# Optimization experiments

Hardware: AMD Instinct MI355X
Metric: run time of the kernel (lower is better)

## Reference

```python
import jax, jax.numpy as jnp
import numpy as np

N, K, M, DIN, DOUT = 4096, 16, 65536, 256, 256


def setup_inputs() -> dict:
    key = jax.random.key(0)
    ks = jax.random.split(key, 16)
    s = 1.0 / np.sqrt(DOUT)
    x = jax.random.normal(ks[0], (N, DIN), jnp.float32)
    h_tensor = jax.random.normal(ks[1], (M, DOUT), jnp.float32)
    c_tensor = jax.random.normal(ks[2], (M, DOUT), jnp.float32)
    # variable-length child lists: lengths in [1, K], -1 padding like get_nums()
    lengths = jax.random.randint(ks[3], (N,), 1, K + 1)
    idx = jax.random.randint(ks[4], (N, K), 0, M)
    t = jnp.arange(K)[None, :]
    indice = jnp.where(t < lengths[:, None], idx, -1).astype(jnp.int32)
    W_w = jax.random.normal(ks[5], (4 * DOUT, DIN), jnp.float32) * s
    W_b = jax.random.normal(ks[6], (4 * DOUT,), jnp.float32) * s
    h0 = jax.random.normal(ks[7], (4, DOUT), jnp.float32)
    c0 = jax.random.normal(ks[8], (4, DOUT), jnp.float32)
    Wih = jax.random.normal(ks[9], (4, 2, 4 * DOUT, DOUT), jnp.float32) * s
    Whh = jax.random.normal(ks[10], (4, 2, 4 * DOUT, DOUT), jnp.float32) * s
    bih = jax.random.normal(ks[11], (4, 2, 4 * DOUT), jnp.float32) * s
    bhh = jax.random.normal(ks[12], (4, 2, 4 * DOUT), jnp.float32) * s
    fc = jax.random.normal(ks[13], (4, DOUT, 2 * DOUT), jnp.float32) * s
    return dict(x=x, h_tensor=h_tensor, c_tensor=c_tensor, indice=indice,
                W_w=W_w, W_b=W_b, h0=h0, c0=c0, Wih=Wih, Whh=Whh,
                bih=bih, bhh=bhh, fc=fc)


def _lstm_dir(xseq, mask, h_init, c_init, W_ih, W_hh, b, reverse):
    """Masked LSTM over child axis. xseq [N,K,d], mask [N,K] bool. Mimics
    pack_padded_sequence: state frozen and output 0 at padded steps."""
    d = h_init.shape[-1]
    xs = jnp.swapaxes(xseq, 0, 1)   # [K,N,d]
    ms = jnp.swapaxes(mask, 0, 1)   # [K,N]

    def step(carry, inp):
        h, c = carry
        xt, mt = inp
        g = xt @ W_ih.T + h @ W_hh.T + b        # [N,4d], gate order i,f,g,o
        i = jax.nn.sigmoid(g[:, :d])
        f = jax.nn.sigmoid(g[:, d:2 * d])
        u = jnp.tanh(g[:, 2 * d:3 * d])
        o = jax.nn.sigmoid(g[:, 3 * d:])
        c_new = f * c + i * u
        h_new = o * jnp.tanh(c_new)
        m = mt[:, None]
        return (jnp.where(m, h_new, h), jnp.where(m, c_new, c)), jnp.where(m, h_new, 0.0)

    _, ys = jax.lax.scan(step, (h_init, c_init), (xs, ms), reverse=reverse)
    return jnp.swapaxes(ys, 0, 1)   # [N,K,d]


def _bilstm_seq(xseq, mask, h0j, c0j, Wihj, Whhj, bihj, bhhj, fcj):
    n = xseq.shape[0]
    h_init = jnp.broadcast_to(h0j, (n, h0j.shape[-1]))
    c_init = jnp.broadcast_to(c0j, (n, c0j.shape[-1]))
    yf = _lstm_dir(xseq, mask, h_init, c_init, Wihj[0], Whhj[0], bihj[0] + bhhj[0], False)
    yb = _lstm_dir(xseq, mask, h_init, c_init, Wihj[1], Whhj[1], bihj[1] + bhhj[1], True)
    y = jnp.concatenate([yf, yb], axis=-1)      # [N,K,2d]
    return jnp.einsum('nkh,dh->nkd', y, fcj)    # fc (no bias); 0 stays 0 at pads


def reference(x, h_tensor, c_tensor, indice, W_w, W_b, h0, c0, Wih, Whh, bih, bhh, fc):
    mask = indice != -1                           # [N,K]
    length = mask.sum(axis=1)                     # [N], >= 1
    safe_idx = jnp.where(mask, indice, 0)
    h = h_tensor[safe_idx]                        # [N,K,d] gather of child states
    c = c_tensor[safe_idx]
    Wx = x @ W_w.T + W_b                          # [N,4d]
    d = DOUT
    Wf, Wi, Wu, Wo = Wx[:, :d], Wx[:, d:2 * d], Wx[:, 2 * d:3 * d], Wx[:, 3 * d:]
    ys = [_bilstm_seq(h, mask, h0[j], c0[j], Wih[j], Whh[j], bih[j], bhh[j], fc[j])
          for j in range(4)]                      # U_f, U_i, U_u, U_o
    # forget branch: per-child gate, masked sum over children
    branch_f_k = jax.nn.sigmoid(Wf[:, None, :] + ys[0])
    branch_f = jnp.sum(branch_f_k * c * mask[..., None], axis=1)
    # i/u/o use last valid timestep (packed LSTM y_last)
    ar = jnp.arange(x.shape[0])
    last = length - 1
    branch_i = jax.nn.sigmoid(ys[1][ar, last] + Wi)
    branch_u = jnp.tanh(ys[2][ar, last] + Wu)
    branch_o = jax.nn.sigmoid(ys[3][ar, last] + Wo)
    new_c = branch_i * branch_u + branch_f
    new_h = branch_o * jnp.tanh(new_c)
    return new_h, new_c
```

## Files before the change

kernel.cpp:

```cpp
#include <hip/hip_runtime.h>
#include <math.h>

#define N_SEQ 4096
#define KCH   16
#define DM    256
#define G4    1024
#define LP    40
#define EP    68

typedef __attribute__((ext_vector_type(8))) short bf8;
typedef __attribute__((ext_vector_type(4))) float f4;

__device__ __forceinline__ float fast_rcp(float x) { return __builtin_amdgcn_rcpf(x); }
__device__ __forceinline__ float sigf(float x)   { return fast_rcp(1.f + __expf(-x)); }
__device__ __forceinline__ float tanh_f(float x) { return 1.f - 2.f * fast_rcp(1.f + __expf(2.f * x)); }

__device__ __forceinline__ float bf2f(unsigned short u) {
    return __uint_as_float(((unsigned)u) << 16);
}
__device__ __forceinline__ unsigned short f2bf(float f) {
    unsigned u = __float_as_uint(f);
    unsigned r = (u + 0x7fffu + ((u >> 16) & 1u)) >> 16;
    return (unsigned short)r;
}
__device__ __forceinline__ unsigned pack2(float a, float b) {
    return (unsigned)f2bf(a) | ((unsigned)f2bf(b) << 16);
}

#define GLDS(gp, lp) __builtin_amdgcn_global_load_lds( \
    (const __attribute__((address_space(1))) void*)(gp), \
    (__attribute__((address_space(3))) void*)(lp), 16, 0, 0)

template<int NSEG, int LDB>
__device__ __forceinline__ void pass_pipe(
    const unsigned short* const (&segA)[NSEG],
    const unsigned short* const (&segB)[NSEG],
    unsigned short* SM,
    f4 (&acc)[4][4], int wave, int wm, int wn, int jq, int fr)
{
    unsigned short* const la[2] = { SM + wave * 1024,        SM + 8192 + wave * 1024 };
    unsigned short* const lb[2] = { SM + 4096 + wave * 1024, SM + 12288 + wave * 1024 };
    constexpr int NS = NSEG * 8;

    {
        const unsigned short* A_ = segA[0];
        const unsigned short* B_ = segB[0];
        GLDS(A_, la[0]);             GLDS(A_ + 16 * DM, la[0] + 512);
        GLDS(B_, lb[0]);             GLDS(B_ + 16 * LDB, lb[0] + 512);
    }
#pragma unroll
    for (int t = 0; t < NS; ++t) {
        if (t + 1 < NS) {
            const unsigned short* A_ = segA[(t + 1) >> 3] + ((t + 1) & 7) * 32;
            const unsigned short* B_ = segB[(t + 1) >> 3] + ((t + 1) & 7) * 32;
            const int nb = (t + 1) & 1;
            GLDS(A_, la[nb]);        GLDS(A_ + 16 * DM, la[nb] + 512);
            GLDS(B_, lb[nb]);        GLDS(B_ + 16 * LDB, lb[nb] + 512);
            asm volatile("s_waitcnt vmcnt(4)" ::: "memory");
        } else {
            asm volatile("s_waitcnt vmcnt(0)" ::: "memory");
        }
        __builtin_amdgcn_s_barrier();

        const unsigned short* Ab = SM + (t & 1) * 8192;
        const unsigned short* Bb = Ab + 4096;
        bf8 af[4], bb[4];
#pragma unroll
        for (int i = 0; i < 4; ++i)
            af[i] = *(const bf8*)(Ab + (wm + i * 16 + fr) * 32 + jq);
#pragma unroll
        for (int j = 0; j < 4; ++j)
            bb[j] = *(const bf8*)(Bb + (wn + j * 16 + fr) * 32 + jq);
#pragma unroll
        for (int i = 0; i < 4; ++i)
#pragma unroll
            for (int j = 0; j < 4; ++j)
                acc[i][j] = __builtin_amdgcn_mfma_f32_16x16x32_bf16(
                    af[i], bb[j], acc[i][j], 0, 0, 0);

        asm volatile("s_waitcnt lgkmcnt(0)" ::: "memory");
        __builtin_amdgcn_s_barrier();
    }
}

template<int KLEN>
__device__ __forceinline__ void pass_bf(
    const unsigned short* __restrict__ aRow,
    const unsigned short* __restrict__ bRow,
    unsigned short* Asm, unsigned short* Bsm, f4 (&acc)[4][4])
{
    const int tid  = threadIdx.x;
    const int kh   = (tid & 1) * 16;
    const int srow = tid >> 1;
    const int lane = tid & 63, wave = tid >> 6;
    const int wm = (wave >> 1) * 64, wn = (wave & 1) * 64;
    const int fr = lane & 15, fk = (lane >> 4) * 8;
    unsigned short* da = Asm + srow * LP + kh;
    unsigned short* db = Bsm + srow * LP + kh;

    for (int k0 = 0; k0 < KLEN; k0 += 32) {
        __syncthreads();
        *(int4*)(da)     = *(const int4*)(aRow + k0 + kh);
        *(int4*)(da + 8) = *(const int4*)(aRow + k0 + kh + 8);
        *(int4*)(db)     = *(const int4*)(bRow + k0 + kh);
        *(int4*)(db + 8) = *(const int4*)(bRow + k0 + kh + 8);
        __syncthreads();
        bf8 af[4], bb[4];
#pragma unroll
        for (int i = 0; i < 4; ++i)
            af[i] = *(const bf8*)(Asm + (wm + i * 16 + fr) * LP + fk);
#pragma unroll
        for (int j = 0; j < 4; ++j)
            bb[j] = *(const bf8*)(Bsm + (wn + j * 16 + fr) * LP + fk);
#pragma unroll
        for (int i = 0; i < 4; ++i)
#pragma unroll
            for (int j = 0; j < 4; ++j)
                acc[i][j] = __builtin_amdgcn_mfma_f32_16x16x32_bf16(
                    af[i], bb[j], acc[i][j], 0, 0, 0);
    }
}

template<int KLEN>
__device__ __forceinline__ void pass_f32(
    const float* __restrict__ aRow,
    const unsigned short* __restrict__ bRow,
    unsigned short* Asm, unsigned short* Bsm, f4 (&acc)[4][4])
{
    const int tid  = threadIdx.x;
    const int kh   = (tid & 1) * 16;
    const int srow = tid >> 1;
    const int lane = tid & 63, wave = tid >> 6;
    const int wm = (wave >> 1) * 64, wn = (wave & 1) * 64;
    const int fr = lane & 15, fk = (lane >> 4) * 8;
    unsigned short* da = Asm + srow * LP + kh;
    unsigned short* db = Bsm + srow * LP + kh;

    for (int k0 = 0; k0 < KLEN; k0 += 32) {
        __syncthreads();
        {
            const float* s = aRow + k0 + kh;
            float4 v0 = *(const float4*)(s);
            float4 v1 = *(const float4*)(s + 4);
            float4 v2 = *(const float4*)(s + 8);
            float4 v3 = *(const float4*)(s + 12);
            *(int4*)(da)     = make_int4(pack2(v0.x, v0.y), pack2(v0.z, v0.w),
                                         pack2(v1.x, v1.y), pack2(v1.z, v1.w));
            *(int4*)(da + 8) = make_int4(pack2(v2.x, v2.y), pack2(v2.z, v2.w),
                                         pack2(v3.x, v3.y), pack2(v3.z, v3.w));
        }
        *(int4*)(db)     = *(const int4*)(bRow + k0 + kh);
        *(int4*)(db + 8) = *(const int4*)(bRow + k0 + kh + 8);
        __syncthreads();
        bf8 af[4], bb[4];
#pragma unroll
        for (int i = 0; i < 4; ++i)
            af[i] = *(const bf8*)(Asm + (wm + i * 16 + fr) * LP + fk);
#pragma unroll
        for (int j = 0; j < 4; ++j)
            bb[j] = *(const bf8*)(Bsm + (wn + j * 16 + fr) * LP + fk);
#pragma unroll
        for (int i = 0; i < 4; ++i)
#pragma unroll
            for (int j = 0; j < 4; ++j)
                acc[i][j] = __builtin_amdgcn_mfma_f32_16x16x32_bf16(
                    af[i], bb[j], acc[i][j], 0, 0, 0);
    }
}


__global__ __launch_bounds__(256) void k_lastidx(
    const int* __restrict__ indice, int* __restrict__ last_idx)
{
    const int n = blockIdx.x * 256 + threadIdx.x;
    if (n >= N_SEQ) return;
    int len = 0;
#pragma unroll
    for (int k = 0; k < KCH; ++k) len += (indice[n * KCH + k] != -1);
    last_idx[n] = indice[n * KCH + (len - 1)];
}

__global__ __launch_bounds__(1024) void k_hh0_bsum2(
    const float* __restrict__ bih, const float* __restrict__ bhh,
    const float* __restrict__ h0, const float* __restrict__ Whh,
    float* __restrict__ bsum2)
{
    const int jz = blockIdx.x, j = jz + 1;
    const int g = threadIdx.x;
    const int jd = j * 2 + 1;
    const float* wrow = Whh + ((size_t)jd * G4 + g) * DM;
    float s = bih[jd * G4 + g] + bhh[jd * G4 + g];
    for (int h = 0; h < DM; ++h) s = fmaf(h0[j * DM + h], wrow[h], s);
    const int c = (g & 255) * 4 + (g >> 8);
    bsum2[jz * G4 + c] = s;
}

__global__ __launch_bounds__(256) void k_init_states(
    const float* __restrict__ h0, const float* __restrict__ c0,
    unsigned short* __restrict__ hA, float* __restrict__ c_state)
{
    const int row = blockIdx.x;
    const int s = row >> 12;
    const int tree = (s < 4) ? s : 0;
    const int d = threadIdx.x;
    hA[(size_t)row * DM + d]      = f2bf(h0[tree * DM + d]);
    c_state[(size_t)row * DM + d] = c0[tree * DM + d];
}

__global__ __launch_bounds__(256) void k_zero4(float4* __restrict__ p)
{
    p[(size_t)blockIdx.x * 256 + threadIdx.x] = make_float4(0.f, 0.f, 0.f, 0.f);
}

__global__ __launch_bounds__(256) void k_prep_wcat(
    const float* __restrict__ Wih, const float* __restrict__ Whh,
    const float* __restrict__ bih, const float* __restrict__ bhh,
    unsigned short* __restrict__ wcat, float* __restrict__ bsumr)
{
    const int c = blockIdx.x, s = blockIdx.y;
    const int wsel = (s < 4) ? s * 2 : 1;
    const int d = c >> 2, g = c & 3;
    const size_t srcrow = ((size_t)wsel * G4 + g * DM + d) * DM;
    unsigned short* dst = wcat + ((size_t)s * G4 + c) * 512;
    const int t = threadIdx.x;
    dst[t]       = f2bf(Wih[srcrow + t]);
    dst[256 + t] = f2bf(Whh[srcrow + t]);
    if (t == 0)
        bsumr[s * G4 + c] = bih[wsel * G4 + g * DM + d] + bhh[wsel * G4 + g * DM + d];
}

__global__ __launch_bounds__(256) void k_prep_wcat2(
    const float* __restrict__ Wih, unsigned short* __restrict__ wcat2)
{
    const int c = blockIdx.x, jz = blockIdx.y, j = jz + 1;
    const int d = c >> 2, g = c & 3;
    const size_t srcrow = ((size_t)(j * 2 + 1) * G4 + g * DM + d) * DM;
    wcat2[((size_t)jz * G4 + c) * 256 + threadIdx.x] = f2bf(Wih[srcrow + threadIdx.x]);
}

__global__ __launch_bounds__(256) void k_prep_fcb(
    const float* __restrict__ fc, unsigned short* __restrict__ fcb)
{
    const int dout = blockIdx.x, z = blockIdx.y, t = threadIdx.x;
    fcb[((size_t)z * DM + dout) * DM + t] = f2bf(fc[(size_t)dout * 512 + z * DM + t]);
}

__global__ __launch_bounds__(256) void k_prep_fcb2(
    const float* __restrict__ fc, unsigned short* __restrict__ fcb2)
{
    const int dout = blockIdx.x, jz = blockIdx.y, j = jz + 1, t = threadIdx.x;
    const float* src = fc + ((size_t)j * DM + dout) * 512;
    unsigned short* dst = fcb2 + ((size_t)jz * DM + dout) * 512;
    dst[t]       = f2bf(src[t]);
    dst[t + 256] = f2bf(src[t + 256]);
}

__global__ __launch_bounds__(256) void k_prep_wwb(
    const float* __restrict__ W_w, unsigned short* __restrict__ wwb)
{
    const size_t i = (size_t)blockIdx.x * 256 + threadIdx.x;
    wwb[i] = f2bf(W_w[i]);
}

__device__ __forceinline__ void gather_slice(
    const float* __restrict__ h_tensor, const int* __restrict__ indice,
    unsigned short* __restrict__ xbuf, int zz, int kk, int blk)
{
    const int row = blk * 64 + (threadIdx.x >> 2);
    const int cb  = (threadIdx.x & 3) * 64;
    int idx = indice[row * KCH + kk]; if (idx < 0) idx = 0;
    const float* src = h_tensor + (size_t)idx * DM + cb;
    unsigned short* dst = xbuf + ((size_t)zz * N_SEQ + row) * DM + cb;
#pragma unroll
    for (int c = 0; c < 64; c += 4) {
        float4 v = *(const float4*)(src + c);
        *(uint2*)(dst + c) = make_uint2(pack2(v.x, v.y), pack2(v.z, v.w));
    }
}

__global__ __launch_bounds__(256) void k_gather_x0(
    const float* __restrict__ h_tensor, const int* __restrict__ indice,
    unsigned short* __restrict__ xbuf)
{
    const int slice = blockIdx.x >> 6, blk = blockIdx.x & 63;
    gather_slice(h_tensor, indice, xbuf, slice, slice ? (KCH - 1) : 0, blk);
}

__global__ __launch_bounds__(256) void k_scan_merged(
    const unsigned short* __restrict__ xb_cur, unsigned short* __restrict__ xb_nxt,
    const unsigned short* __restrict__ yb_prev, unsigned short* __restrict__ yb_cur,
    const int* __restrict__ indice, const float* __restrict__ h_tensor,
    const unsigned short* __restrict__ h_in, unsigned short* __restrict__ h_out,
    float* __restrict__ c_state,
    const unsigned short* __restrict__ wcat, const float* __restrict__ bsumr,
    const unsigned short* __restrict__ fcb, unsigned short* __restrict__ ys0,
    int r)
{
    __shared__ __align__(16) unsigned short SMEM[16384];

    const int tid  = threadIdx.x;
    const int lane = tid & 63, wave = tid >> 6;
    const int wm = (wave >> 1) * 64, wn = (wave & 1) * 64;
    const int fr = lane & 15;
    const int jq = ((lane >> 4) ^ ((fr >> 1) & 3)) * 8;
    const int lr = wave * 32 + (lane >> 2);
    const int jl = ((lane & 3) ^ ((lane >> 3) & 3)) * 8;

    const int bz = blockIdx.z;

    if (bz == 5) {
        const int id5 = blockIdx.x + 8 * blockIdx.y;
        if (id5 >= 128) {
            const int rr = r + 1;
            if (rr >= KCH) return;
            const int g = id5 - 128;
            const int zz = g >> 6;
            gather_slice(h_tensor, indice, xb_nxt, zz,
                         zz ? (KCH - 1 - rr) : rr, g & 63);
            return;
        }
        if (r == 0) return;
        const int rp = r - 1;
        const int z = id5 >> 6;
        const int kslice = z ? (KCH - 1 - rp) : rp;
        const int row0 = (id5 & 31) * 128;
        const int c0 = ((id5 >> 5) & 1) * 128;

        const unsigned short* ay0 = yb_prev + ((size_t)z * N_SEQ + row0 + lr) * DM + jl;
        const unsigned short* bf0 = fcb + ((size_t)z * DM + c0 + lr) * DM + jl;

        f4 acc[4][4];
#pragma unroll
        for (int i = 0; i < 4; ++i)
#pragma unroll
            for (int j = 0; j < 4; ++j) acc[i][j] = (f4)(0.f);
        {
            const unsigned short* const segA[1] = { ay0 };
            const unsigned short* const segB[1] = { bf0 };
            pass_pipe<1, 256>(segA, segB, SMEM, acc, wave, wm, wn, jq, fr);
        }

#pragma unroll
        for (int i = 0; i < 4; ++i)
#pragma unroll
            for (int j = 0; j < 4; ++j) {
                const int col = c0 + wn + j * 16 + fr;
#pragma unroll
                for (int reg = 0; reg < 4; ++reg) {
                    const int rowg = row0 + wm + i * 16 + (lane >> 4) * 4 + reg;
                    const size_t ix = ((size_t)rowg * KCH + kslice) * DM + col;
                    ys0[ix] = f2bf(bf2f(ys0[ix]) + acc[i][j][reg]);
                }
            }
        return;
    }

    const int s = bz;
    const int k = (s < 4) ? r : (KCH - 1 - r);
    const int z = (s < 4) ? 0 : 1;
    const int bn = blockIdx.y & 7;
    const int bm = (blockIdx.y >> 3) * 8 + blockIdx.x;
    const int row0 = bm * 128, c0 = bn * 128;

    const unsigned short* xz = xb_cur + (size_t)z * N_SEQ * DM;
    const unsigned short* hs_in = h_in + (size_t)s * N_SEQ * DM;
    const unsigned short* ax0 = xz + (size_t)(row0 + lr) * DM + jl;
    const unsigned short* ah0 = hs_in + (size_t)(row0 + lr) * DM + jl;
    const unsigned short* bw0 = wcat + ((size_t)s * G4 + c0 + lr) * 512 + jl;

    f4 acc[4][4];
#pragma unroll
    for (int i = 0; i < 4; ++i)
#pragma unroll
        for (int j = 0; j < 4; ++j) acc[i][j] = (f4)(0.f);

    {
        const unsigned short* const segA[2] = { ax0, ah0 };
        const unsigned short* const segB[2] = { bw0, bw0 + 256 };
        pass_pipe<2, 512>(segA, segB, SMEM, acc, wave, wm, wn, jq, fr);
    }

    float* sc = (float*)SMEM + wave * (16 * EP);
    __syncthreads();
#pragma unroll
    for (int i = 0; i < 4; ++i) {
#pragma unroll
        for (int j = 0; j < 4; ++j) {
            const int colL = j * 16 + fr;
            const int rbase = (lane >> 4) * 4;
#pragma unroll
            for (int reg = 0; reg < 4; ++reg)
                sc[(rbase + reg) * EP + colL] = acc[i][j][reg];
        }
        __syncthreads();
        const int rowg = row0 + wm + i * 16 + fr;
        const bool m = (indice[rowg * KCH + k] != -1);
#pragma unroll
        for (int q = 0; q < 4; ++q) {
            const int dL = (lane >> 4) + q * 4;
            const f4 gv = *(const f4*)(sc + fr * EP + dL * 4);
            const f4 bb = *(const f4*)(bsumr + s * G4 + c0 + wn + dL * 4);
            const int d = ((c0 + wn) >> 2) + dL;
            const float ii = sigf(gv.x + bb.x);
            const float ff = sigf(gv.y + bb.y);
            const float uu = tanh_f(gv.z + bb.z);
            const float oo = sigf(gv.w + bb.w);
            const size_t cix = ((size_t)s * N_SEQ + rowg) * DM + d;
            const float c_old = c_state[cix];
            const float cn = ff * c_old + ii * uu;
            const float cw = m ? cn : c_old;
            c_state[cix] = cw;
            const float hn = oo * tanh_f(cn);
            const unsigned short hv = m ? f2bf(hn) : hs_in[(size_t)rowg * DM + d];
            h_out[cix] = hv;
            if (s == 0)
                yb_cur[(size_t)rowg * DM + d] = m ? f2bf(hn) : (unsigned short)0;
            else if (s == 4)
                yb_cur[(size_t)(N_SEQ + rowg) * DM + d] = m ? f2bf(hn) : (unsigned short)0;
        }
        __syncthreads();
    }
}

__global__ __launch_bounds__(256) void k_acc_tail(
    const unsigned short* __restrict__ ybuf, const unsigned short* __restrict__ fcb,
    unsigned short* __restrict__ ys0)
{
    __shared__ __align__(16) unsigned short SMEM[16384];
    const int tid = threadIdx.x;
    const int lane = tid & 63, wave = tid >> 6;
    const int wm = (wave >> 1) * 64, wn = (wave & 1) * 64;
    const int fr = lane & 15;
    const int jq = ((lane >> 4) ^ ((fr >> 1) & 3)) * 8;
    const int lr = wave * 32 + (lane >> 2);
    const int jl = ((lane & 3) ^ ((lane >> 3) & 3)) * 8;

    const int z = blockIdx.z;
    const int kslice = z ? 0 : (KCH - 1);
    const int row0 = blockIdx.y * 128, c0 = blockIdx.x * 128;

    const unsigned short* ay0 = ybuf + ((size_t)z * N_SEQ + row0 + lr) * DM + jl;
    const unsigned short* bf0 = fcb + ((size_t)z * DM + c0 + lr) * DM + jl;

    f4 acc[4][4];
#pragma unroll
    for (int i = 0; i < 4; ++i)
#pragma unroll
        for (int j = 0; j < 4; ++j) acc[i][j] = (f4)(0.f);
    {
        const unsigned short* const segA[1] = { ay0 };
        const unsigned short* const segB[1] = { bf0 };
        pass_pipe<1, 256>(segA, segB, SMEM, acc, wave, wm, wn, jq, fr);
    }

#pragma unroll
    for (int i = 0; i < 4; ++i)
#pragma unroll
        for (int j = 0; j < 4; ++j) {
            const int col = c0 + wn + j * 16 + fr;
#pragma unroll
            for (int reg = 0; reg < 4; ++reg) {
                const int rowg = row0 + wm + i * 16 + (lane >> 4) * 4 + reg;
                const size_t ix = ((size_t)rowg * KCH + kslice) * DM + col;
                ys0[ix] = f2bf(bf2f(ys0[ix]) + acc[i][j][reg]);
            }
        }
}


__global__ __launch_bounds__(256) void k_bwd_mfma(
    const float* __restrict__ h_tensor, const int* __restrict__ last_idx,
    const unsigned short* __restrict__ wcat2, const float* __restrict__ bsum2,
    const float* __restrict__ c0, unsigned short* __restrict__ yb_last)
{
    __shared__ __align__(16) unsigned short SMEM[2 * 128 * LP];
    const int jz = blockIdx.z, j = jz + 1;
    const int row0 = blockIdx.y * 128, c0t = blockIdx.x * 128;
    const int tid = threadIdx.x;
    const int srow = tid >> 1;

    const float* aF = h_tensor + (size_t)last_idx[row0 + srow] * DM;
    const unsigned short* bR = wcat2 + ((size_t)jz * G4 + c0t + srow) * 256;

    f4 acc[4][4];
#pragma unroll
    for (int i = 0; i < 4; ++i)
#pragma unroll
        for (int jj = 0; jj < 4; ++jj) acc[i][jj] = (f4)(0.f);

    pass_f32<256>(aF, bR, SMEM, SMEM + 128 * LP, acc);

    const int lane = tid & 63, wave = tid >> 6;
    const int wm = (wave >> 1) * 64, wn = (wave & 1) * 64;
    float* sc = (float*)SMEM + wave * (16 * EP);

    __syncthreads();
#pragma unroll
    for (int i = 0; i < 4; ++i) {
#pragma unroll
        for (int jj = 0; jj < 4; ++jj) {
            const int colL = jj * 16 + (lane & 15);
            const int rbase = (lane >> 4) * 4;
#pragma unroll
            for (int reg = 0; reg < 4; ++reg)
                sc[(rbase + reg) * EP + colL] = acc[i][jj][reg];
        }
        __syncthreads();
        const int rowg = row0 + wm + i * 16 + (lane & 15);
#pragma unroll
        for (int q = 0; q < 4; ++q) {
            const int dL = (lane >> 4) + q * 4;
            const f4 gv = *(const f4*)(sc + (lane & 15) * EP + dL * 4);
            const f4 bb = *(const f4*)(bsum2 + jz * G4 + c0t + wn + dL * 4);
            const int d = ((c0t + wn) >> 2) + dL;
            const float ii = sigf(gv.x + bb.x);
            const float ff = sigf(gv.y + bb.y);
            const float uu = tanh_f(gv.z + bb.z);
            const float oo = sigf(gv.w + bb.w);
            const float cn = ff * c0[j * DM + d] + ii * uu;
            yb_last[((size_t)jz * N_SEQ + rowg) * DM + d] = f2bf(oo * tanh_f(cn));
        }
        __syncthreads();
    }
}

__global__ __launch_bounds__(256) void k_wx_mfma(
    const float* __restrict__ x, const unsigned short* __restrict__ wwb,
    const float* __restrict__ W_b, unsigned short* __restrict__ Wx)
{
    __shared__ __align__(16) unsigned short SMEM[2 * 128 * LP];
    const int row0 = blockIdx.y * 128, c0 = blockIdx.x * 128;
    const int tid = threadIdx.x;
    const int srow = tid >> 1;

    const float* aF = x + (size_t)(row0 + srow) * DM;
    const unsigned short* bR = wwb + (size_t)(c0 + srow) * DM;

    f4 acc[4][4];
#pragma unroll
    for (int i = 0; i < 4; ++i)
#pragma unroll
        for (int j = 0; j < 4; ++j) acc[i][j] = (f4)(0.f);

    pass_f32<256>(aF, bR, SMEM, SMEM + 128 * LP, acc);

    const int lane = tid & 63, wave = tid >> 6;
    const int wm = (wave >> 1) * 64, wn = (wave & 1) * 64;
#pragma unroll
    for (int i = 0; i < 4; ++i)
#pragma unroll
        for (int j = 0; j < 4; ++j) {
            const int col = c0 + wn + j * 16 + (lane & 15);
            const float bv = W_b[col];
#pragma unroll
            for (int reg = 0; reg < 4; ++reg) {
                const int rowg = row0 + wm + i * 16 + (lane >> 4) * 4 + reg;
                Wx[(size_t)rowg * G4 + col] = f2bf(acc[i][j][reg] + bv);
            }
        }
}

__global__ __launch_bounds__(256) void k_fc_last_mfma(
    const unsigned short* __restrict__ h_final, const unsigned short* __restrict__ yb_last,
    const unsigned short* __restrict__ fcb2, unsigned short* __restrict__ ys_last)
{
    __shared__ __align__(16) unsigned short SMEM[2 * 128 * LP];
    const int jz = blockIdx.z;
    const int row0 = blockIdx.y * 128, c0 = blockIdx.x * 128;
    const int tid = threadIdx.x;
    const int srow = tid >> 1;

    const unsigned short* aH1 = h_final + ((size_t)(1 + jz) * N_SEQ + row0 + srow) * DM;
    const unsigned short* aH2 = yb_last + ((size_t)jz * N_SEQ + row0 + srow) * DM;
    const unsigned short* bR  = fcb2 + ((size_t)jz * DM + c0 + srow) * 512;

    f4 acc[4][4];
#pragma unroll
    for (int i = 0; i < 4; ++i)
#pragma unroll
        for (int j = 0; j < 4; ++j) acc[i][j] = (f4)(0.f);

    pass_bf<256>(aH1, bR, SMEM, SMEM + 128 * LP, acc);
    pass_bf<256>(aH2, bR + 256, SMEM, SMEM + 128 * LP, acc);

    const int lane = tid & 63, wave = tid >> 6;
    const int wm = (wave >> 1) * 64, wn = (wave & 1) * 64;
#pragma unroll
    for (int i = 0; i < 4; ++i)
#pragma unroll
        for (int j = 0; j < 4; ++j) {
            const int col = c0 + wn + j * 16 + (lane & 15);
#pragma unroll
            for (int reg = 0; reg < 4; ++reg) {
                const int rowg = row0 + wm + i * 16 + (lane >> 4) * 4 + reg;
                ys_last[((size_t)jz * N_SEQ + rowg) * DM + col] = f2bf(acc[i][j][reg]);
            }
        }
}

__global__ __launch_bounds__(256) void k_final(
    const unsigned short* __restrict__ Wx, const unsigned short* __restrict__ ys0,
    const unsigned short* __restrict__ ys_last, const float* __restrict__ c_tensor,
    const int* __restrict__ indice, float* __restrict__ out)
{
    const int n = blockIdx.x, d = threadIdx.x;
    const float Wf = bf2f(Wx[(size_t)n * G4 + d]);
    const float Wi = bf2f(Wx[(size_t)n * G4 + DM + d]);
    const float Wu = bf2f(Wx[(size_t)n * G4 + 2 * DM + d]);
    const float Wo = bf2f(Wx[(size_t)n * G4 + 3 * DM + d]);
    float bf = 0.f;
#pragma unroll
    for (int k = 0; k < KCH; ++k) {
        const int id = indice[n * KCH + k];
        if (id >= 0)
            bf += sigf(Wf + bf2f(ys0[((size_t)n * KCH + k) * DM + d])) *
                  c_tensor[(size_t)id * DM + d];
    }
    const float bi = sigf(bf2f(ys_last[((size_t)0 * N_SEQ + n) * DM + d]) + Wi);
    const float bu = tanh_f(bf2f(ys_last[((size_t)1 * N_SEQ + n) * DM + d]) + Wu);
    const float bo = sigf(bf2f(ys_last[((size_t)2 * N_SEQ + n) * DM + d]) + Wo);
    const float nc = bi * bu + bf;
    const float nh = bo * tanh_f(nc);
    out[(size_t)n * DM + d] = nh;
    out[(size_t)N_SEQ * DM + (size_t)n * DM + d] = nc;
}

extern "C" void kernel_launch(void* const* d_in, const int* in_sizes, int n_in,
                              void* d_out, int out_size, void* d_ws, size_t ws_size,
                              hipStream_t stream)
{
    const float* x        = (const float*)d_in[0];
    const float* h_tensor = (const float*)d_in[1];
    const float* c_tensor = (const float*)d_in[2];
    const int*   indice   = (const int*)d_in[3];
    const float* W_w      = (const float*)d_in[4];
    const float* W_b      = (const float*)d_in[5];
    const float* h0       = (const float*)d_in[6];
    const float* c0       = (const float*)d_in[7];
    const float* Wih      = (const float*)d_in[8];
    const float* Whh      = (const float*)d_in[9];
    const float* bih      = (const float*)d_in[10];
    const float* bhh      = (const float*)d_in[11];
    const float* fc       = (const float*)d_in[12];
    float* out = (float*)d_out;

    char* base = (char*)d_ws;
    float*          c_state  = (float*)(base + 0);
    int*            last_idx = (int*)  (base + 20971520);
    float*          bsumr    = (float*)(base + 20987904);
    unsigned short* hA       = (unsigned short*)(base + 21008384);
    unsigned short* hB       = (unsigned short*)(base + 31494144);
    unsigned short* ys0      = (unsigned short*)(base + 41979904);
    unsigned short* ybufA    = (unsigned short*)(base + 75534336);
    unsigned short* ybufB    = (unsigned short*)(base + 79728640);
    unsigned short* xbufA    = (unsigned short*)(base + 83922944);
    unsigned short* fcb      = (unsigned short*)(base + 88117248);
    unsigned short* postbuf  = (unsigned short*)(base + 88379392);
    unsigned short* wcat     = (unsigned short*)(base + 92573696);
    const size_t need = 97816576;
    if (ws_size < need) return;

    unsigned short* xbufB   = postbuf;
    unsigned short* wcat2   = postbuf;
    unsigned short* fcb2    = postbuf + 786432;
    unsigned short* wwb     = postbuf + 1179648;
    float*          bsum2   = (float*)(postbuf + 1441792);
    unsigned short* yb_last = ybufA;
    unsigned short* ys_last = hB;
    unsigned short* WxBuf   = hA;

    k_lastidx<<<16, 256, 0, stream>>>(indice, last_idx);
    k_init_states<<<5 * N_SEQ, 256, 0, stream>>>(h0, c0, hA, c_state);
    k_zero4<<<8192, 256, 0, stream>>>((float4*)ys0);
    k_prep_wcat<<<dim3(G4, 5), 256, 0, stream>>>(Wih, Whh, bih, bhh, wcat, bsumr);
    k_prep_fcb<<<dim3(DM, 2), 256, 0, stream>>>(fc, fcb);
    k_gather_x0<<<128, 256, 0, stream>>>(h_tensor, indice, xbufA);

    for (int r = 0; r < KCH; ++r) {
        const unsigned short* xb_cur = (r & 1) ? xbufB : xbufA;
        unsigned short* xb_nxt       = (r & 1) ? xbufA : xbufB;
        const unsigned short* yb_prev = (r & 1) ? ybufA : ybufB;
        unsigned short* yb_cur        = (r & 1) ? ybufB : ybufA;
        const unsigned short* h_in = (r & 1) ? hB : hA;
        unsigned short* h_out      = (r & 1) ? hA : hB;
        k_scan_merged<<<dim3(8, 32, 6), 256, 0, stream>>>(
            xb_cur, xb_nxt, yb_prev, yb_cur, indice, h_tensor,
            h_in, h_out, c_state, wcat, bsumr, fcb, ys0, r);
    }

    k_acc_tail<<<dim3(2, 32, 2), 256, 0, stream>>>(ybufB, fcb, ys0);

    k_prep_wcat2<<<dim3(G4, 3), 256, 0, stream>>>(Wih, wcat2);
    k_hh0_bsum2<<<3, 1024, 0, stream>>>(bih, bhh, h0, Whh, bsum2);
    k_prep_fcb2<<<dim3(DM, 3), 256, 0, stream>>>(fc, fcb2);
    k_prep_wwb<<<1024, 256, 0, stream>>>(W_w, wwb);

    k_bwd_mfma<<<dim3(8, 32, 3), 256, 0, stream>>>(
        h_tensor, last_idx, wcat2, bsum2, c0, yb_last);
    k_fc_last_mfma<<<dim3(2, 32, 3), 256, 0, stream>>>(hA, yb_last, fcb2, ys_last);
    k_wx_mfma<<<dim3(8, 32), 256, 0, stream>>>(x, wwb, W_b, WxBuf);

    k_final<<<N_SEQ, 256, 0, stream>>>(WxBuf, ys0, ys_last, c_tensor, indice, out);
}
```

Before: 1.390 ms.

## Triple-buffer LDS pipeline with prefetch distance two, drop trailing barrier

Converts the double-buffered global_load_lds pipeline into a three-stage ring with loads issued two steps ahead, removing the per-step trailing lgkmcnt wait and barrier. MFMA sections are wrapped in s_setprio to favour matrix issue. The epilogue's __syncthreads around the per-wave scratch area are replaced by an LDS wait plus a sched_barrier, since each wave uses its own region. LDS grows by half in the kernels that call the pipeline, which may reduce occupancy, and the scratch region must not alias buffers still being filled.

```diff
diff --git a/kernel.cpp b/kernel.cpp
--- a/kernel.cpp
+++ b/kernel.cpp
@@ -38,31 +38,41 @@
     unsigned short* SM,
     f4 (&acc)[4][4], int wave, int wm, int wn, int jq, int fr)
 {
-    unsigned short* const la[2] = { SM + wave * 1024,        SM + 8192 + wave * 1024 };
-    unsigned short* const lb[2] = { SM + 4096 + wave * 1024, SM + 12288 + wave * 1024 };
     constexpr int NS = NSEG * 8;
 
     {
-        const unsigned short* A_ = segA[0];
-        const unsigned short* B_ = segB[0];
-        GLDS(A_, la[0]);             GLDS(A_ + 16 * DM, la[0] + 512);
-        GLDS(B_, lb[0]);             GLDS(B_ + 16 * LDB, lb[0] + 512);
+        const unsigned short* A0 = segA[0];
+        const unsigned short* B0 = segB[0];
+        unsigned short* a = SM + wave * 1024;
+        unsigned short* b = SM + 4096 + wave * 1024;
+        GLDS(A0, a);            GLDS(A0 + 16 * DM, a + 512);
+        GLDS(B0, b);            GLDS(B0 + 16 * LDB, b + 512);
+        const unsigned short* A1 = segA[0] + 32;
+        const unsigned short* B1 = segB[0] + 32;
+        a = SM + 8192 + wave * 1024;
+        b = SM + 8192 + 4096 + wave * 1024;
+        GLDS(A1, a);            GLDS(A1 + 16 * DM, a + 512);
+        GLDS(B1, b);            GLDS(B1 + 16 * LDB, b + 512);
     }
 #pragma unroll
     for (int t = 0; t < NS; ++t) {
-        if (t + 1 < NS) {
-            const unsigned short* A_ = segA[(t + 1) >> 3] + ((t + 1) & 7) * 32;
-            const unsigned short* B_ = segB[(t + 1) >> 3] + ((t + 1) & 7) * 32;
-            const int nb = (t + 1) & 1;
-            GLDS(A_, la[nb]);        GLDS(A_ + 16 * DM, la[nb] + 512);
-            GLDS(B_, lb[nb]);        GLDS(B_ + 16 * LDB, lb[nb] + 512);
+        if (t < NS - 1)
             asm volatile("s_waitcnt vmcnt(4)" ::: "memory");
-        } else {
+        else
             asm volatile("s_waitcnt vmcnt(0)" ::: "memory");
-        }
         __builtin_amdgcn_s_barrier();
 
-        const unsigned short* Ab = SM + (t & 1) * 8192;
+        if (t + 2 < NS) {
+            const int tn = t + 2;
+            const unsigned short* A_ = segA[tn >> 3] + (tn & 7) * 32;
+            const unsigned short* B_ = segB[tn >> 3] + (tn & 7) * 32;
+            unsigned short* a = SM + (tn % 3) * 8192 + wave * 1024;
+            unsigned short* b = a + 4096;
+            GLDS(A_, a);        GLDS(A_ + 16 * DM, a + 512);
+            GLDS(B_, b);        GLDS(B_ + 16 * LDB, b + 512);
+        }
+
+        const unsigned short* Ab = SM + (t % 3) * 8192;
         const unsigned short* Bb = Ab + 4096;
         bf8 af[4], bb[4];
 #pragma unroll
@@ -71,15 +81,15 @@
 #pragma unroll
         for (int j = 0; j < 4; ++j)
             bb[j] = *(const bf8*)(Bb + (wn + j * 16 + fr) * 32 + jq);
+
+        __builtin_amdgcn_s_setprio(1);
 #pragma unroll
         for (int i = 0; i < 4; ++i)
 #pragma unroll
             for (int j = 0; j < 4; ++j)
                 acc[i][j] = __builtin_amdgcn_mfma_f32_16x16x32_bf16(
                     af[i], bb[j], acc[i][j], 0, 0, 0);
-
-        asm volatile("s_waitcnt lgkmcnt(0)" ::: "memory");
-        __builtin_amdgcn_s_barrier();
+        __builtin_amdgcn_s_setprio(0);
     }
 }
 
@@ -296,7 +306,7 @@
     const unsigned short* __restrict__ fcb, unsigned short* __restrict__ ys0,
     int r)
 {
-    __shared__ __align__(16) unsigned short SMEM[16384];
+    __shared__ __align__(16) unsigned short SMEM[24576];
 
     const int tid  = threadIdx.x;
     const int lane = tid & 63, wave = tid >> 6;
@@ -392,7 +402,8 @@
             for (int reg = 0; reg < 4; ++reg)
                 sc[(rbase + reg) * EP + colL] = acc[i][j][reg];
         }
-        __syncthreads();
+        asm volatile("s_waitcnt lgkmcnt(0)" ::: "memory");
+        __builtin_amdgcn_sched_barrier(0);
         const int rowg = row0 + wm + i * 16 + fr;
         const bool m = (indice[rowg * KCH + k] != -1);
 #pragma unroll
@@ -418,7 +429,8 @@
             else if (s == 4)
                 yb_cur[(size_t)(N_SEQ + rowg) * DM + d] = m ? f2bf(hn) : (unsigned short)0;
         }
-        __syncthreads();
+        asm volatile("s_waitcnt lgkmcnt(0)" ::: "memory");
+        __builtin_amdgcn_sched_barrier(0);
     }
 }
 
@@ -426,7 +438,7 @@
     const unsigned short* __restrict__ ybuf, const unsigned short* __restrict__ fcb,
     unsigned short* __restrict__ ys0)
 {
-    __shared__ __align__(16) unsigned short SMEM[16384];
+    __shared__ __align__(16) unsigned short SMEM[24576];
     const int tid = threadIdx.x;
     const int lane = tid & 63, wave = tid >> 6;
     const int wm = (wave >> 1) * 64, wn = (wave & 1) * 64;
```

Measured after the change: 1.298 ms. -6.6%, faster.
